# Performance work log

Measured on AMD Instinct MI355X. Metric: run time of the kernel, lower is better.

Reference implementation:

```python
import jax, jax.numpy as jnp
import numpy as np

N = 100000       # nodes
E = 1200000      # edges (before self loops)
IN = 3
H = 64           # hidden
HNUM = 256       # number of direct virtual nodes
L = 2            # layers - 1 (hidden GATConvs and VN MLPs)
NEG_SLOPE = 0.2  # GATConv default


def setup_inputs() -> dict:
    key = jax.random.key(0)
    ks = jax.random.split(key, 20)
    s_in = 1.0 / np.sqrt(IN)
    s_h = 1.0 / np.sqrt(H)
    inp = dict(
        x=jax.random.normal(ks[0], (N, IN), dtype=jnp.float32),
        edge_index=jax.random.randint(ks[1], (2, E), 0, N, dtype=jnp.int32),
        h_blocks=jax.random.randint(ks[2], (N,), 0, HNUM, dtype=jnp.int32),
        h_levels=jax.random.randint(ks[3], (N,), 0, 4, dtype=jnp.int32),
        h_num=HNUM,
        # initial GATConv(IN -> H)
        w_in=jax.random.normal(ks[4], (IN, H), dtype=jnp.float32) * s_in,
        a_src_in=jax.random.normal(ks[5], (H,), dtype=jnp.float32) * s_h,
        a_dst_in=jax.random.normal(ks[6], (H,), dtype=jnp.float32) * s_h,
        b_in=jnp.zeros((H,), dtype=jnp.float32),
        # L hidden GATConv(H -> H) layers, stacked
        w_l=jax.random.normal(ks[7], (L, H, H), dtype=jnp.float32) * s_h,
        a_src_l=jax.random.normal(ks[8], (L, H), dtype=jnp.float32) * s_h,
        a_dst_l=jax.random.normal(ks[9], (L, H), dtype=jnp.float32) * s_h,
        b_l=jnp.zeros((L, H), dtype=jnp.float32),
        # L virtual-node MLPs: Linear-ReLU-Linear-ReLU
        mlp_w1=jax.random.normal(ks[10], (L, H, H), dtype=jnp.float32) * s_h,
        mlp_b1=jnp.zeros((L, H), dtype=jnp.float32),
        mlp_w2=jax.random.normal(ks[11], (L, H, H), dtype=jnp.float32) * s_h,
        mlp_b2=jnp.zeros((L, H), dtype=jnp.float32),
        # virtualnode embedding, constant-initialized to 0 in original
        vn_emb=jnp.zeros((1, H), dtype=jnp.float32),
    )
    return inp


def _gat_conv(x, src, dst, n, W, a_src, a_dst, b):
    """PyG GATConv, heads=1, add_self_loops already in (src,dst)."""
    h = x @ W                                   # [n, H]
    alpha = jax.nn.leaky_relu((h @ a_src)[src] + (h @ a_dst)[dst], NEG_SLOPE)
    # softmax over incoming edges of each dst node (self-loops => nonempty)
    amax = jax.ops.segment_max(alpha, dst, num_segments=n)
    ex = jnp.exp(alpha - amax[dst])
    denom = jax.ops.segment_sum(ex, dst, num_segments=n)
    w = ex / denom[dst]                         # [E_total]
    out = jax.ops.segment_sum(w[:, None] * h[src], dst, num_segments=n)
    return out + b


def _mlp(v, w1, b1, w2, b2):
    return jax.nn.relu(jax.nn.relu(v @ w1 + b1) @ w2 + b2)


def reference(x, edge_index, h_blocks, h_levels, h_num,
              w_in, a_src_in, a_dst_in, b_in,
              w_l, a_src_l, a_dst_l, b_l,
              mlp_w1, mlp_b1, mlp_w2, mlp_b2, vn_emb):
    n = x.shape[0]
    loops = jnp.arange(n, dtype=edge_index.dtype)
    src = jnp.concatenate([edge_index[0], loops])
    dst = jnp.concatenate([edge_index[1], loops])

    out = _gat_conv(x, src, dst, n, w_in, a_src_in, a_dst_in, b_in)
    vn_direct = jnp.broadcast_to(vn_emb, (h_num, vn_emb.shape[1]))  # zeros init
    vn_root = vn_emb                                                # [1, H]

    for l in range(L):
        out = out + vn_direct[h_blocks]
        out = _gat_conv(out, src, dst, n, w_l[l], a_src_l[l], a_dst_l[l], b_l[l])
        vn_direct = jax.ops.segment_sum(out, h_blocks, num_segments=h_num) + vn_direct
        vn_direct = vn_direct + vn_root
        vn_root = jnp.sum(vn_direct, axis=0, keepdims=True) + vn_root
        # original applies ALL vn MLPs each layer (faithful reproduction)
        for m in range(L):
            vn_direct = _mlp(vn_direct, mlp_w1[m], mlp_b1[m], mlp_w2[m], mlp_b2[m])
            vn_root = _mlp(vn_root, mlp_w1[m], mlp_b1[m], mlp_w2[m], mlp_b2[m])
    return out
```

## Files before the change

kernel.cpp:

```cpp
#include <hip/hip_runtime.h>


typedef __attribute__((ext_vector_type(8))) short short8;
typedef __attribute__((ext_vector_type(4))) float f32x4;

__device__ __forceinline__ unsigned short f2bf(float x){
    unsigned u = __float_as_uint(x);
    unsigned r = (u + 0x7fffu + ((u >> 16) & 1u)) >> 16;
    return (unsigned short)r;
}
__device__ __forceinline__ float bf2f(unsigned short b){
    return __uint_as_float(((unsigned)b) << 16);
}

#define BSHIFT 9
#define CHUNK 4096
#define NSLICE 8

__device__ __forceinline__ int incl_scan256(int v, int* sums4){
    int lane = threadIdx.x & 63, w = threadIdx.x >> 6;
    int x = v;
    #pragma unroll
    for (int o = 1; o < 64; o <<= 1){ int t = __shfl_up(x, o, 64); if (lane >= o) x += t; }
    __syncthreads();
    if (lane == 63) sums4[w] = x;
    __syncthreads();
    for (int j = 0; j < w; ++j) x += sums4[j];
    return x;
}

__global__ __launch_bounds__(256) void k_bucket_count(const int* __restrict__ dst, int E, int NB,
                                                      int* __restrict__ bucketCount){
    __shared__ int cnt[256];
    cnt[threadIdx.x] = 0;
    __syncthreads();
    int base = blockIdx.x*CHUNK;
    int lim = min(base + CHUNK, E);
    for (int i = base + threadIdx.x; i < lim; i += 256)
        atomicAdd(&cnt[dst[i] >> BSHIFT], 1);
    __syncthreads();
    if (threadIdx.x < NB && cnt[threadIdx.x])
        atomicAdd(&bucketCount[threadIdx.x], cnt[threadIdx.x]);
}

__global__ __launch_bounds__(256) void k_hb_count(const int* __restrict__ hb, int N,
                                                  int* __restrict__ hbBins){
    __shared__ int cnt[256];
    cnt[threadIdx.x] = 0;
    __syncthreads();
    int base = blockIdx.x*CHUNK;
    int lim = min(base + CHUNK, N);
    for (int i = base + threadIdx.x; i < lim; i += 256)
        atomicAdd(&cnt[hb[i]], 1);
    __syncthreads();
    if (cnt[threadIdx.x])
        atomicAdd(&hbBins[threadIdx.x], cnt[threadIdx.x]);
}

__global__ __launch_bounds__(256) void k_scan_all(const int* __restrict__ bucketCount,
                                                  int NB, int E, int N,
                                                  int* __restrict__ bucketOff,
                                                  int* __restrict__ bucketCur,
                                                  int* __restrict__ rowptr,
                                                  const int* __restrict__ hbBins,
                                                  int* __restrict__ binptr,
                                                  int* __restrict__ bincur){
    __shared__ int sums4[4];
    int tid = threadIdx.x;
    int v = (tid < NB) ? bucketCount[tid] : 0;
    int x = incl_scan256(v, sums4);
    if (tid < NB){ bucketOff[tid] = x - v; bucketCur[tid] = x - v; }
    if (tid == NB-1) bucketOff[NB] = x;
    if (tid == 0) rowptr[N] = E;
    int v2 = hbBins[tid];
    int x2 = incl_scan256(v2, sums4);
    binptr[tid] = x2 - v2;
    bincur[tid] = x2 - v2;
    if (tid == 255) binptr[256] = x2;
}

__global__ __launch_bounds__(256) void k_bucket_place(const int* __restrict__ src,
                                                      const int* __restrict__ dst, int E, int NB,
                                                      int* __restrict__ bucketCur,
                                                      int2* __restrict__ pairs){
    __shared__ int cnt[256], binStart[256], binCur[256], chunkBase[256];
    __shared__ int sums4[4];
    __shared__ int2 lp[CHUNK];
    int tid = threadIdx.x;
    cnt[tid] = 0; binCur[tid] = 0;
    __syncthreads();
    int base = blockIdx.x*CHUNK;
    int s[16], d[16];
    #pragma unroll
    for (int k = 0; k < 16; ++k){
        int i = base + k*256 + tid;
        if (i < E){ s[k] = src[i]; d[k] = dst[i]; atomicAdd(&cnt[d[k] >> BSHIFT], 1); }
        else d[k] = -1;
    }
    __syncthreads();
    int v = cnt[tid];
    int x = incl_scan256(v, sums4);
    binStart[tid] = x - v;
    __syncthreads();
    #pragma unroll
    for (int k = 0; k < 16; ++k){
        if (d[k] >= 0){
            int b = d[k] >> BSHIFT;
            int p = binStart[b] + atomicAdd(&binCur[b], 1);
            lp[p] = make_int2(s[k], d[k]);
        }
    }
    if (tid < NB){
        int c = cnt[tid];
        chunkBase[tid] = c ? atomicAdd(&bucketCur[tid], c) : 0;
    }
    __syncthreads();
    int total = min(CHUNK, E - base);
    for (int i = tid; i < total; i += 256){
        int2 p = lp[i];
        int b = p.y >> BSHIFT;
        pairs[chunkBase[b] + (i - binStart[b])] = p;
    }
}

__global__ __launch_bounds__(256) void k_hb_place(const int* __restrict__ hb, int N,
                                                  int* __restrict__ bincur,
                                                  int* __restrict__ nodes){
    __shared__ int cnt[256], binStart[256], binCur[256], chunkBase[256];
    __shared__ int sums4[4];
    __shared__ int lp[CHUNK];
    __shared__ unsigned char lb[CHUNK];
    int tid = threadIdx.x;
    cnt[tid] = 0; binCur[tid] = 0;
    __syncthreads();
    int base = blockIdx.x*CHUNK;
    int key[16];
    #pragma unroll
    for (int k = 0; k < 16; ++k){
        int i = base + k*256 + tid;
        key[k] = (i < N) ? hb[i] : -1;
        if (key[k] >= 0) atomicAdd(&cnt[key[k]], 1);
    }
    __syncthreads();
    int v = cnt[tid];
    int x = incl_scan256(v, sums4);
    binStart[tid] = x - v;
    __syncthreads();
    #pragma unroll
    for (int k = 0; k < 16; ++k){
        if (key[k] >= 0){
            int p = binStart[key[k]] + atomicAdd(&binCur[key[k]], 1);
            lp[p] = base + k*256 + tid;
            lb[p] = (unsigned char)key[k];
        }
    }
    if (cnt[tid]) chunkBase[tid] = atomicAdd(&bincur[tid], cnt[tid]);
    __syncthreads();
    int total = min(CHUNK, N - base);
    for (int i = tid; i < total; i += 256){
        int b = lb[i];
        nodes[chunkBase[b] + (i - binStart[b])] = lp[i];
    }
}

__global__ __launch_bounds__(256) void k_bucket_csr(const int2* __restrict__ pairs,
                                                    const int* __restrict__ bucketOff, int N,
                                                    int* __restrict__ rowptr,
                                                    int* __restrict__ colarr){
    __shared__ int deg[512], cur[512];
    __shared__ int sums4[4];
    __shared__ int tAs;
    int b = blockIdx.x, tid = threadIdx.x;
    int d0 = b << BSHIFT;
    int e0 = bucketOff[b], e1 = bucketOff[b+1];
    deg[tid] = 0; deg[256+tid] = 0;
    __syncthreads();
    for (int i = e0 + tid; i < e1; i += 256)
        atomicAdd(&deg[pairs[i].y - d0], 1);
    __syncthreads();
    int vA = deg[tid], vB = deg[256+tid];
    int xA = incl_scan256(vA, sums4);
    if (tid == 255) tAs = xA;
    int xB = incl_scan256(vB, sums4) + tAs;
    int exclA = xA - vA, exclB = xB - vB;
    cur[tid] = exclA; cur[256+tid] = exclB;
    int dA = d0 + tid, dB = d0 + 256 + tid;
    if (dA < N) rowptr[dA] = e0 + exclA;
    if (dB < N) rowptr[dB] = e0 + exclB;
    __syncthreads();
    for (int i = e0 + tid; i < e1; i += 256){
        int2 p = pairs[i];
        int pos = e0 + atomicAdd(&cur[p.y - d0], 1);
        colarr[pos] = p.x;
    }
}

__global__ __launch_bounds__(256) void k_transform_in(const float* __restrict__ x,
                                                      const float* __restrict__ W,
                                                      const float* __restrict__ a_src,
                                                      const float* __restrict__ a_dst,
                                                      unsigned short* __restrict__ hout,
                                                      float* __restrict__ ssrc,
                                                      float* __restrict__ sdst, int N){
    int wv = blockIdx.x*4 + (threadIdx.x >> 6);
    int lane = threadIdx.x & 63;
    if (wv >= N) return;
    float acc = 0.f;
    #pragma unroll
    for (int k = 0; k < 3; ++k)
        acc += x[wv*3 + k] * W[k*64 + lane];
    hout[(size_t)wv*64 + lane] = f2bf(acc);
    float v1 = acc * a_src[lane];
    float v2 = acc * a_dst[lane];
    #pragma unroll
    for (int o = 32; o; o >>= 1){ v1 += __shfl_xor(v1, o, 64); v2 += __shfl_xor(v2, o, 64); }
    if (lane == 0){ ssrc[wv] = v1; sdst[wv] = v2; }
}

#define LDW 72
__global__ __launch_bounds__(256) void k_transform_h_mfma(const float* __restrict__ feat,
                                                          const float* __restrict__ vn,
                                                          const float* __restrict__ vn_emb,
                                                          const int* __restrict__ hb,
                                                          const float* __restrict__ W,
                                                          const float* __restrict__ a_src,
                                                          const float* __restrict__ a_dst,
                                                          unsigned short* __restrict__ hout,
                                                          float* __restrict__ ssrc,
                                                          float* __restrict__ sdst, int N){
    __shared__ unsigned short WhT[64*LDW], WlT[64*LDW], Ah[64*LDW], Al[64*LDW];
    const int n0 = blockIdx.x * 64;

    for (int idx = threadIdx.x; idx < 4096; idx += 256){
        int n = idx >> 6, k = idx & 63;
        float w = W[k*64 + n];
        unsigned short hi = f2bf(w);
        WhT[n*LDW + k] = hi;
        WlT[n*LDW + k] = f2bf(w - bf2f(hi));
    }
    for (int t = threadIdx.x; t < 1024; t += 256){
        int row = t >> 4, c4 = t & 15;
        int node = n0 + row;
        float4 v = make_float4(0.f,0.f,0.f,0.f);
        if (node < N){
            v = ((const float4*)feat)[(size_t)node*16 + c4];
            float4 g = vn ? ((const float4*)vn)[(size_t)hb[node]*16 + c4]
                          : ((const float4*)vn_emb)[c4];
            v.x += g.x; v.y += g.y; v.z += g.z; v.w += g.w;
        }
        int base = row*LDW + c4*4;
        unsigned short h0 = f2bf(v.x), h1 = f2bf(v.y), h2 = f2bf(v.z), h3 = f2bf(v.w);
        Ah[base+0] = h0; Al[base+0] = f2bf(v.x - bf2f(h0));
        Ah[base+1] = h1; Al[base+1] = f2bf(v.y - bf2f(h1));
        Ah[base+2] = h2; Al[base+2] = f2bf(v.z - bf2f(h2));
        Ah[base+3] = h3; Al[base+3] = f2bf(v.w - bf2f(h3));
    }
    __syncthreads();

    int lane = threadIdx.x & 63;
    int wv   = threadIdx.x >> 6;
    int mrow = lane & 15, quad = lane >> 4;
    int m0 = wv * 16;

    f32x4 acc0 = {0,0,0,0}, acc1 = {0,0,0,0}, acc2 = {0,0,0,0}, acc3 = {0,0,0,0};
    #pragma unroll
    for (int k0 = 0; k0 < 64; k0 += 32){
        int kb = k0 + quad*8;
        short8 ah = *(const short8*)&Ah[(m0+mrow)*LDW + kb];
        short8 al = *(const short8*)&Al[(m0+mrow)*LDW + kb];
        short8 b0h = *(const short8*)&WhT[( 0+mrow)*LDW + kb];
        short8 b1h = *(const short8*)&WhT[(16+mrow)*LDW + kb];
        short8 b2h = *(const short8*)&WhT[(32+mrow)*LDW + kb];
        short8 b3h = *(const short8*)&WhT[(48+mrow)*LDW + kb];
        short8 b0l = *(const short8*)&WlT[( 0+mrow)*LDW + kb];
        short8 b1l = *(const short8*)&WlT[(16+mrow)*LDW + kb];
        short8 b2l = *(const short8*)&WlT[(32+mrow)*LDW + kb];
        short8 b3l = *(const short8*)&WlT[(48+mrow)*LDW + kb];
        acc0 = __builtin_amdgcn_mfma_f32_16x16x32_bf16(ah, b0h, acc0, 0, 0, 0);
        acc1 = __builtin_amdgcn_mfma_f32_16x16x32_bf16(ah, b1h, acc1, 0, 0, 0);
        acc2 = __builtin_amdgcn_mfma_f32_16x16x32_bf16(ah, b2h, acc2, 0, 0, 0);
        acc3 = __builtin_amdgcn_mfma_f32_16x16x32_bf16(ah, b3h, acc3, 0, 0, 0);
        acc0 = __builtin_amdgcn_mfma_f32_16x16x32_bf16(ah, b0l, acc0, 0, 0, 0);
        acc1 = __builtin_amdgcn_mfma_f32_16x16x32_bf16(ah, b1l, acc1, 0, 0, 0);
        acc2 = __builtin_amdgcn_mfma_f32_16x16x32_bf16(ah, b2l, acc2, 0, 0, 0);
        acc3 = __builtin_amdgcn_mfma_f32_16x16x32_bf16(ah, b3l, acc3, 0, 0, 0);
        acc0 = __builtin_amdgcn_mfma_f32_16x16x32_bf16(al, b0h, acc0, 0, 0, 0);
        acc1 = __builtin_amdgcn_mfma_f32_16x16x32_bf16(al, b1h, acc1, 0, 0, 0);
        acc2 = __builtin_amdgcn_mfma_f32_16x16x32_bf16(al, b2h, acc2, 0, 0, 0);
        acc3 = __builtin_amdgcn_mfma_f32_16x16x32_bf16(al, b3h, acc3, 0, 0, 0);
    }

    float as0 = a_src[mrow], as1 = a_src[16+mrow], as2 = a_src[32+mrow], as3 = a_src[48+mrow];
    float ad0 = a_dst[mrow], ad1 = a_dst[16+mrow], ad2 = a_dst[32+mrow], ad3 = a_dst[48+mrow];
    #pragma unroll
    for (int r = 0; r < 4; ++r){
        float p1 = acc0[r]*as0 + acc1[r]*as1 + acc2[r]*as2 + acc3[r]*as3;
        float p2 = acc0[r]*ad0 + acc1[r]*ad1 + acc2[r]*ad2 + acc3[r]*ad3;
        #pragma unroll
        for (int o = 8; o; o >>= 1){ p1 += __shfl_xor(p1, o, 64); p2 += __shfl_xor(p2, o, 64); }
        int node = n0 + m0 + quad*4 + r;
        if (mrow == 0 && node < N){ ssrc[node] = p1; sdst[node] = p2; }
    }
    #pragma unroll
    for (int r = 0; r < 4; ++r){
        int row = m0 + quad*4 + r;
        Ah[row*LDW + mrow     ] = f2bf(acc0[r]);
        Ah[row*LDW + mrow + 16] = f2bf(acc1[r]);
        Ah[row*LDW + mrow + 32] = f2bf(acc2[r]);
        Ah[row*LDW + mrow + 48] = f2bf(acc3[r]);
    }
    int r2 = lane >> 2, seg = lane & 3;
    int node = n0 + m0 + r2;
    if (node < N){
        short8 va = *(const short8*)&Ah[(m0+r2)*LDW + seg*16];
        short8 vb = *(const short8*)&Ah[(m0+r2)*LDW + seg*16 + 8];
        *(short8*)&hout[(size_t)node*64 + seg*16]     = va;
        *(short8*)&hout[(size_t)node*64 + seg*16 + 8] = vb;
    }
}

__global__ __launch_bounds__(256) void k_aggregate(const unsigned short* __restrict__ h,
                                                   const float* __restrict__ ssrc,
                                                   const float* __restrict__ sdst,
                                                   const int* __restrict__ rowptr,
                                                   const int* __restrict__ col,
                                                   const float* __restrict__ bias,
                                                   float* __restrict__ out, int N){
    __shared__ float2 swb[4][64];
    int wv = threadIdx.x >> 6;
    int d = blockIdx.x*4 + wv;
    int lane = threadIdx.x & 63;
    if (d >= N) return;
    int q = lane >> 4, c4 = lane & 15;
    float sd = sdst[d];
    float a0 = ssrc[d] + sd; a0 = (a0 < 0.f) ? 0.2f*a0 : a0;
    float dlocal = 0.f;
    float4 acc = make_float4(0.f,0.f,0.f,0.f);
    if (q == 0){
        uint2 u = *(const uint2*)&h[(size_t)d*64 + c4*4];
        acc.x = __uint_as_float(u.x << 16);
        acc.y = __uint_as_float(u.x & 0xffff0000u);
        acc.z = __uint_as_float(u.y << 16);
        acc.w = __uint_as_float(u.y & 0xffff0000u);
    }
    int e0 = rowptr[d], e1 = rowptr[d+1];
    for (int base = e0; base < e1; base += 64){
        int ne = min(64, e1 - base);
        float w = 0.f; int s = 0;
        if (lane < ne){
            s = col[base + lane];
            float a = ssrc[s] + sd; a = (a < 0.f) ? 0.2f*a : a;
            w = __expf(a - a0);
        }
        dlocal += w;
        swb[wv][lane] = make_float2(w, __int_as_float(s));
        for (int j = 0; j < ne; j += 4){
            float2 p = swb[wv][j + q];
            int sj = __float_as_int(p.y);
            uint2 u = *(const uint2*)&h[(size_t)sj*64 + c4*4];
            acc.x += p.x * __uint_as_float(u.x << 16);
            acc.y += p.x * __uint_as_float(u.x & 0xffff0000u);
            acc.z += p.x * __uint_as_float(u.y << 16);
            acc.w += p.x * __uint_as_float(u.y & 0xffff0000u);
        }
    }
    #pragma unroll
    for (int o = 32; o; o >>= 1) dlocal += __shfl_xor(dlocal, o, 64);
    float denom = 1.0f + dlocal;
    #pragma unroll
    for (int o = 16; o <= 32; o <<= 1){
        acc.x += __shfl_xor(acc.x, o, 64);
        acc.y += __shfl_xor(acc.y, o, 64);
        acc.z += __shfl_xor(acc.z, o, 64);
        acc.w += __shfl_xor(acc.w, o, 64);
    }
    if (q == 0){
        float4 b4 = ((const float4*)bias)[c4];
        float inv = 1.0f/denom;
        ((float4*)out)[(size_t)d*16 + c4] =
            make_float4(acc.x*inv + b4.x, acc.y*inv + b4.y,
                        acc.z*inv + b4.z, acc.w*inv + b4.w);
    }
}

__global__ __launch_bounds__(256) void k_vn_segsum2(const float* __restrict__ outA,
                                                    const int* __restrict__ nodes,
                                                    const int* __restrict__ binptr,
                                                    float* __restrict__ vseg){
    __shared__ float part[4][64];
    int b = blockIdx.x >> 3, s = blockIdx.x & (NSLICE-1);
    int wv = threadIdx.x >> 6, lane = threadIdx.x & 63;
    int i0 = binptr[b], i1 = binptr[b+1];
    int len = i1 - i0;
    int lo = i0 + (len*s)/NSLICE;
    int hi = i0 + (len*(s+1))/NSLICE;
    float acc = 0.f;
    for (int i = lo + wv; i < hi; i += 4){
        int n = nodes[i];
        acc += outA[(size_t)n*64 + lane];
    }
    part[wv][lane] = acc;
    __syncthreads();
    if (threadIdx.x < 64)
        vseg[(size_t)blockIdx.x*64 + lane] =
            part[0][lane] + part[1][lane] + part[2][lane] + part[3][lane];
}

__global__ __launch_bounds__(256) void k_vn_combine(const float* __restrict__ vseg,
                                                    const float* __restrict__ vd_old,
                                                    const float* __restrict__ root_old,
                                                    const float* __restrict__ vn_emb,
                                                    float* __restrict__ vw){
    __shared__ float part[4][64];
    int wv = threadIdx.x >> 6, lane = threadIdx.x & 63;
    float rold = root_old ? root_old[lane] : vn_emb[lane];
    float emb  = vn_emb[lane];
    float csum = 0.f;
    for (int b = wv*64; b < wv*64 + 64; ++b){
        float v = 0.f;
        #pragma unroll
        for (int s = 0; s < NSLICE; ++s)
            v += vseg[(size_t)(b*NSLICE + s)*64 + lane];
        v += (vd_old ? vd_old[b*64 + lane] : emb) + rold;
        vw[b*64 + lane] = v;
        csum += v;
    }
    part[wv][lane] = csum;
    __syncthreads();
    if (threadIdx.x < 64)
        vw[256*64 + lane] = part[0][lane] + part[1][lane] + part[2][lane] + part[3][lane] + rold;
}

__global__ __launch_bounds__(256) void k_vn_mlp(const float* __restrict__ mlp_w1,
                                                const float* __restrict__ mlp_b1,
                                                const float* __restrict__ mlp_w2,
                                                const float* __restrict__ mlp_b2,
                                                int L, float* __restrict__ vw){
    __shared__ float Wl[64*64];
    int wv = blockIdx.x*4 + (threadIdx.x >> 6);
    int lane = threadIdx.x & 63;
    bool valid = (wv < 257);
    float iv = valid ? vw[wv*64 + lane] : 0.f;
    for (int m = 0; m < L; ++m){
        #pragma unroll
        for (int half = 0; half < 2; ++half){
            const float* W    = (half ? mlp_w2 : mlp_w1) + (size_t)m*4096;
            const float* bias = (half ? mlp_b2 : mlp_b1) + (size_t)m*64;
            __syncthreads();
            for (int i = threadIdx.x; i < 4096; i += 256) Wl[i] = W[i];
            __syncthreads();
            float acc = bias[lane];
            #pragma unroll
            for (int k = 0; k < 64; ++k)
                acc += __shfl(iv, k, 64) * Wl[k*64 + lane];
            iv = fmaxf(acc, 0.f);
        }
    }
    if (valid) vw[wv*64 + lane] = iv;
}

extern "C" void kernel_launch(void* const* d_in, const int* in_sizes, int n_in,
                              void* d_out, int out_size, void* d_ws, size_t ws_size,
                              hipStream_t stream) {
    const int N = in_sizes[0] / 3;
    const int E = in_sizes[1] / 2;
    const int L = in_sizes[9] / (64*64);
    const int NB = (N + (1<<BSHIFT) - 1) >> BSHIFT;

    const float* x        = (const float*)d_in[0];
    const int*   edge     = (const int*)d_in[1];
    const int*   srcp     = edge;
    const int*   dstp     = edge + E;
    const int*   hb       = (const int*)d_in[2];
    const float* w_in     = (const float*)d_in[5];
    const float* a_src_in = (const float*)d_in[6];
    const float* a_dst_in = (const float*)d_in[7];
    const float* b_in     = (const float*)d_in[8];
    const float* w_l      = (const float*)d_in[9];
    const float* a_src_l  = (const float*)d_in[10];
    const float* a_dst_l  = (const float*)d_in[11];
    const float* b_l      = (const float*)d_in[12];
    const float* mlp_w1   = (const float*)d_in[13];
    const float* mlp_b1   = (const float*)d_in[14];
    const float* mlp_w2   = (const float*)d_in[15];
    const float* mlp_b2   = (const float*)d_in[16];
    const float* vn_emb   = (const float*)d_in[17];
    float*       out      = (float*)d_out;

    char* ws = (char*)d_ws;
    size_t off = 0;
    auto carve = [&](size_t bytes) -> char* {
        char* p = ws + off;
        off = (off + bytes + 255) & ~(size_t)255;
        return p;
    };
    unsigned short* h = (unsigned short*)carve((size_t)N*64*2);
    float* outA   = (float*)carve((size_t)N*64*4);
    float* ssrc   = (float*)carve((size_t)N*4);
    float* sdst   = (float*)carve((size_t)N*4);
    int*   rowptr = (int*)carve((size_t)(N+1)*4);
    char*  zstart = ws + off;
    int*   bucketCount = (int*)carve(256*4);
    int*   hbBins = (int*)carve(256*4);
    size_t zbytes = (size_t)((ws + off) - zstart);
    int*   bucketOff = (int*)carve(257*4);
    int*   bucketCur = (int*)carve(256*4);
    int*   binptr = (int*)carve(257*4);
    int*   bincur = (int*)carve(256*4);
    int*   colarr = (int*)carve((size_t)E*4);
    int*   nodes  = (int*)carve((size_t)N*4);
    float* vseg   = (float*)carve((size_t)256*NSLICE*64*4);
    float* vw     = (float*)carve((size_t)257*64*4);
    if (off > ws_size) return;
    int2* pairs = (int2*)h;

    hipMemsetAsync(zstart, 0, zbytes, stream);
    const int nchunkE = (E + CHUNK - 1) / CHUNK;
    const int nchunkN = (N + CHUNK - 1) / CHUNK;
    k_bucket_count<<<nchunkE, 256, 0, stream>>>(dstp, E, NB, bucketCount);
    k_hb_count    <<<nchunkN, 256, 0, stream>>>(hb, N, hbBins);
    k_scan_all    <<<1, 256, 0, stream>>>(bucketCount, NB, E, N, bucketOff, bucketCur, rowptr,
                                          hbBins, binptr, bincur);
    k_bucket_place<<<nchunkE, 256, 0, stream>>>(srcp, dstp, E, NB, bucketCur, pairs);
    k_bucket_csr  <<<NB, 256, 0, stream>>>(pairs, bucketOff, N, rowptr, colarr);
    k_hb_place    <<<nchunkN, 256, 0, stream>>>(hb, N, bincur, nodes);

    const int nwb = (N + 3) / 4;
    const int nmb = (N + 63) / 64;

    k_transform_in<<<nwb, 256, 0, stream>>>(x, w_in, a_src_in, a_dst_in, h, ssrc, sdst, N);
    k_aggregate<<<nwb, 256, 0, stream>>>(h, ssrc, sdst, rowptr, colarr, b_in, outA, N);

    for (int l = 0; l < L; ++l){
        const float* vnp = (l == 0) ? nullptr : vw;
        k_transform_h_mfma<<<nmb, 256, 0, stream>>>(outA, vnp, vn_emb, hb,
                                                    w_l + (size_t)l*4096,
                                                    a_src_l + (size_t)l*64,
                                                    a_dst_l + (size_t)l*64,
                                                    h, ssrc, sdst, N);
        const bool last = (l == L-1);
        float* dst_buf = last ? out : outA;
        k_aggregate<<<nwb, 256, 0, stream>>>(h, ssrc, sdst, rowptr, colarr,
                                             b_l + (size_t)l*64, dst_buf, N);
        if (!last){
            const float* vdo = (l == 0) ? nullptr : vw;
            const float* ro  = (l == 0) ? nullptr : (vw + 256*64);
            k_vn_segsum2<<<256*NSLICE, 256, 0, stream>>>(outA, nodes, binptr, vseg);
            k_vn_combine<<<1, 256, 0, stream>>>(vseg, vdo, ro, vn_emb, vw);
            k_vn_mlp<<<(257+3)/4, 256, 0, stream>>>(mlp_w1, mlp_b1, mlp_w2, mlp_b2, L, vw);
        }
    }
}
```

Measured before the change: 420.1 us.

## Pack source attention score into padded bf16 feature rows and widen gather

The per-node source attention score is stored inside a padded 72-element bf16 feature row, so the edge gather reads score and features from one row instead of a separate ssrc array. The aggregate kernel also switches from 16 lanes × 4 features (4 edges at once) to 8 lanes × 8 features with 16-byte loads (8 edges at once). This aims to cut scattered memory transactions per edge. In exchange the feature buffer grows by 12.5%, and the score read touches a different 16-byte segment of the row than the feature reads.

```diff
diff --git a/kernel.cpp b/kernel.cpp
--- a/kernel.cpp
+++ b/kernel.cpp
@@ -16,6 +16,7 @@
 #define BSHIFT 9
 #define CHUNK 4096
 #define NSLICE 8
+#define HROW 72
 
 __device__ __forceinline__ int incl_scan256(int v, int* sums4){
     int lane = threadIdx.x & 63, w = threadIdx.x >> 6;
@@ -200,7 +201,6 @@
                                                       const float* __restrict__ a_src,
                                                       const float* __restrict__ a_dst,
                                                       unsigned short* __restrict__ hout,
-                                                      float* __restrict__ ssrc,
                                                       float* __restrict__ sdst, int N){
     int wv = blockIdx.x*4 + (threadIdx.x >> 6);
     int lane = threadIdx.x & 63;
@@ -209,12 +209,15 @@
     #pragma unroll
     for (int k = 0; k < 3; ++k)
         acc += x[wv*3 + k] * W[k*64 + lane];
-    hout[(size_t)wv*64 + lane] = f2bf(acc);
+    hout[(size_t)wv*HROW + 8 + lane] = f2bf(acc);
     float v1 = acc * a_src[lane];
     float v2 = acc * a_dst[lane];
     #pragma unroll
     for (int o = 32; o; o >>= 1){ v1 += __shfl_xor(v1, o, 64); v2 += __shfl_xor(v2, o, 64); }
-    if (lane == 0){ ssrc[wv] = v1; sdst[wv] = v2; }
+    if (lane == 0){
+        *(float*)&hout[(size_t)wv*HROW] = v1;
+        sdst[wv] = v2;
+    }
 }
 
 #define LDW 72
@@ -226,7 +229,6 @@
                                                           const float* __restrict__ a_src,
                                                           const float* __restrict__ a_dst,
                                                           unsigned short* __restrict__ hout,
-                                                          float* __restrict__ ssrc,
                                                           float* __restrict__ sdst, int N){
     __shared__ unsigned short WhT[64*LDW], WlT[64*LDW], Ah[64*LDW], Al[64*LDW];
     const int n0 = blockIdx.x * 64;
@@ -299,7 +301,10 @@
         #pragma unroll
         for (int o = 8; o; o >>= 1){ p1 += __shfl_xor(p1, o, 64); p2 += __shfl_xor(p2, o, 64); }
         int node = n0 + m0 + quad*4 + r;
-        if (mrow == 0 && node < N){ ssrc[node] = p1; sdst[node] = p2; }
+        if (mrow == 0 && node < N){
+            *(float*)&hout[(size_t)node*HROW] = p1;
+            sdst[node] = p2;
+        }
     }
     #pragma unroll
     for (int r = 0; r < 4; ++r){
@@ -314,13 +319,12 @@
     if (node < N){
         short8 va = *(const short8*)&Ah[(m0+r2)*LDW + seg*16];
         short8 vb = *(const short8*)&Ah[(m0+r2)*LDW + seg*16 + 8];
-        *(short8*)&hout[(size_t)node*64 + seg*16]     = va;
-        *(short8*)&hout[(size_t)node*64 + seg*16 + 8] = vb;
+        *(short8*)&hout[(size_t)node*HROW + 8 + seg*16]     = va;
+        *(short8*)&hout[(size_t)node*HROW + 8 + seg*16 + 8] = vb;
     }
 }
 
 __global__ __launch_bounds__(256) void k_aggregate(const unsigned short* __restrict__ h,
-                                                   const float* __restrict__ ssrc,
                                                    const float* __restrict__ sdst,
                                                    const int* __restrict__ rowptr,
                                                    const int* __restrict__ col,
@@ -331,17 +335,18 @@
     int d = blockIdx.x*4 + wv;
     int lane = threadIdx.x & 63;
     if (d >= N) return;
-    int q = lane >> 4, c4 = lane & 15;
+    int r8 = lane >> 3, c8 = lane & 7;
     float sd = sdst[d];
-    float a0 = ssrc[d] + sd; a0 = (a0 < 0.f) ? 0.2f*a0 : a0;
+    float a0 = *(const float*)&h[(size_t)d*HROW] + sd;
+    a0 = (a0 < 0.f) ? 0.2f*a0 : a0;
     float dlocal = 0.f;
-    float4 acc = make_float4(0.f,0.f,0.f,0.f);
-    if (q == 0){
-        uint2 u = *(const uint2*)&h[(size_t)d*64 + c4*4];
-        acc.x = __uint_as_float(u.x << 16);
-        acc.y = __uint_as_float(u.x & 0xffff0000u);
-        acc.z = __uint_as_float(u.y << 16);
-        acc.w = __uint_as_float(u.y & 0xffff0000u);
+    float acc[8] = {0,0,0,0,0,0,0,0};
+    if (r8 == 0){
+        uint4 u = *(const uint4*)&h[(size_t)d*HROW + 8 + c8*8];
+        acc[0] = __uint_as_float(u.x << 16); acc[1] = __uint_as_float(u.x & 0xffff0000u);
+        acc[2] = __uint_as_float(u.y << 16); acc[3] = __uint_as_float(u.y & 0xffff0000u);
+        acc[4] = __uint_as_float(u.z << 16); acc[5] = __uint_as_float(u.z & 0xffff0000u);
+        acc[6] = __uint_as_float(u.w << 16); acc[7] = __uint_as_float(u.w & 0xffff0000u);
     }
     int e0 = rowptr[d], e1 = rowptr[d+1];
     for (int base = e0; base < e1; base += 64){
@@ -349,37 +354,45 @@
         float w = 0.f; int s = 0;
         if (lane < ne){
             s = col[base + lane];
-            float a = ssrc[s] + sd; a = (a < 0.f) ? 0.2f*a : a;
+            float a = *(const float*)&h[(size_t)s*HROW] + sd;
+            a = (a < 0.f) ? 0.2f*a : a;
             w = __expf(a - a0);
         }
         dlocal += w;
         swb[wv][lane] = make_float2(w, __int_as_float(s));
-        for (int j = 0; j < ne; j += 4){
-            float2 p = swb[wv][j + q];
+        int nj = (ne + 7) >> 3;
+        for (int j = 0; j < nj; ++j){
+            float2 p = swb[wv][j*8 + r8];
             int sj = __float_as_int(p.y);
-            uint2 u = *(const uint2*)&h[(size_t)sj*64 + c4*4];
-            acc.x += p.x * __uint_as_float(u.x << 16);
-            acc.y += p.x * __uint_as_float(u.x & 0xffff0000u);
-            acc.z += p.x * __uint_as_float(u.y << 16);
-            acc.w += p.x * __uint_as_float(u.y & 0xffff0000u);
+            uint4 u = *(const uint4*)&h[(size_t)sj*HROW + 8 + c8*8];
+            acc[0] += p.x * __uint_as_float(u.x << 16);
+            acc[1] += p.x * __uint_as_float(u.x & 0xffff0000u);
+            acc[2] += p.x * __uint_as_float(u.y << 16);
+            acc[3] += p.x * __uint_as_float(u.y & 0xffff0000u);
+            acc[4] += p.x * __uint_as_float(u.z << 16);
+            acc[5] += p.x * __uint_as_float(u.z & 0xffff0000u);
+            acc[6] += p.x * __uint_as_float(u.w << 16);
+            acc[7] += p.x * __uint_as_float(u.w & 0xffff0000u);
         }
     }
     #pragma unroll
     for (int o = 32; o; o >>= 1) dlocal += __shfl_xor(dlocal, o, 64);
     float denom = 1.0f + dlocal;
     #pragma unroll
-    for (int o = 16; o <= 32; o <<= 1){
-        acc.x += __shfl_xor(acc.x, o, 64);
-        acc.y += __shfl_xor(acc.y, o, 64);
-        acc.z += __shfl_xor(acc.z, o, 64);
-        acc.w += __shfl_xor(acc.w, o, 64);
-    }
-    if (q == 0){
-        float4 b4 = ((const float4*)bias)[c4];
+    for (int o = 8; o <= 32; o <<= 1){
+        #pragma unroll
+        for (int k = 0; k < 8; ++k) acc[k] += __shfl_xor(acc[k], o, 64);
+    }
+    if (r8 == 0){
         float inv = 1.0f/denom;
-        ((float4*)out)[(size_t)d*16 + c4] =
-            make_float4(acc.x*inv + b4.x, acc.y*inv + b4.y,
-                        acc.z*inv + b4.z, acc.w*inv + b4.w);
+        float4 b4a = ((const float4*)bias)[c8*2];
+        float4 b4b = ((const float4*)bias)[c8*2 + 1];
+        float4 o1 = make_float4(acc[0]*inv + b4a.x, acc[1]*inv + b4a.y,
+                                acc[2]*inv + b4a.z, acc[3]*inv + b4a.w);
+        float4 o2 = make_float4(acc[4]*inv + b4b.x, acc[5]*inv + b4b.y,
+                                acc[6]*inv + b4b.z, acc[7]*inv + b4b.w);
+        ((float4*)out)[(size_t)d*16 + c8*2    ] = o1;
+        ((float4*)out)[(size_t)d*16 + c8*2 + 1] = o2;
     }
 }
 
@@ -494,9 +507,8 @@
         off = (off + bytes + 255) & ~(size_t)255;
         return p;
     };
-    unsigned short* h = (unsigned short*)carve((size_t)N*64*2);
+    unsigned short* h = (unsigned short*)carve((size_t)N*HROW*2);
     float* outA   = (float*)carve((size_t)N*64*4);
-    float* ssrc   = (float*)carve((size_t)N*4);
     float* sdst   = (float*)carve((size_t)N*4);
     int*   rowptr = (int*)carve((size_t)(N+1)*4);
     char*  zstart = ws + off;
@@ -528,8 +540,8 @@
     const int nwb = (N + 3) / 4;
     const int nmb = (N + 63) / 64;
 
-    k_transform_in<<<nwb, 256, 0, stream>>>(x, w_in, a_src_in, a_dst_in, h, ssrc, sdst, N);
-    k_aggregate<<<nwb, 256, 0, stream>>>(h, ssrc, sdst, rowptr, colarr, b_in, outA, N);
+    k_transform_in<<<nwb, 256, 0, stream>>>(x, w_in, a_src_in, a_dst_in, h, sdst, N);
+    k_aggregate<<<nwb, 256, 0, stream>>>(h, sdst, rowptr, colarr, b_in, outA, N);
 
     for (int l = 0; l < L; ++l){
         const float* vnp = (l == 0) ? nullptr : vw;
@@ -537,10 +549,10 @@
                                                     w_l + (size_t)l*4096,
                                                     a_src_l + (size_t)l*64,
                                                     a_dst_l + (size_t)l*64,
-                                                    h, ssrc, sdst, N);
+                                                    h, sdst, N);
         const bool last = (l == L-1);
         float* dst_buf = last ? out : outA;
-        k_aggregate<<<nwb, 256, 0, stream>>>(h, ssrc, sdst, rowptr, colarr,
+        k_aggregate<<<nwb, 256, 0, stream>>>(h, sdst, rowptr, colarr,
                                              b_l + (size_t)l*64, dst_buf, N);
         if (!last){
             const float* vdo = (l == 0) ? nullptr : vw;
```

Result: slower. 437.7 us (+4.2%).
